# Kernel tuning notes

Hardware: AMD Instinct MI355X
Metric: run time of the kernel (lower is better)

The kernel has to match this reference:

```python
import jax, jax.numpy as jnp
import numpy as np

N_NODE = 100000
N_EDGE = 1600000
D_IN = 128
D_OUT = 128
D_EDGE = 32
EPS = 1e-10


def setup_inputs() -> dict:
    key = jax.random.key(0)
    ks = jax.random.split(key, 8)
    x = jax.random.normal(ks[0], (N_NODE, D_IN), dtype=jnp.float32)
    edge_list = jax.random.randint(ks[1], (N_EDGE, 2), 0, N_NODE, dtype=jnp.int32)
    edge_weights = jax.random.uniform(ks[2], (N_EDGE,), dtype=jnp.float32)
    edge_feature = jax.random.normal(ks[3], (N_EDGE, D_EDGE), dtype=jnp.float32)
    W_lin = jax.random.normal(ks[4], (D_OUT, D_IN), dtype=jnp.float32) * 0.05
    b_lin = jnp.zeros((D_OUT,), dtype=jnp.float32)
    W_edge = jax.random.normal(ks[5], (D_IN, D_EDGE), dtype=jnp.float32) * 0.05
    b_edge = jnp.zeros((D_IN,), dtype=jnp.float32)
    return {"x": x, "edge_list": edge_list, "edge_weights": edge_weights,
            "edge_feature": edge_feature, "W_lin": W_lin, "b_lin": b_lin,
            "W_edge": W_edge, "b_edge": b_edge}


def reference(x, edge_list, edge_weights, edge_feature, W_lin, b_lin, W_edge, b_edge):
    N = x.shape[0]
    src = edge_list[:, 0]  # node_in
    dst = edge_list[:, 1]  # node_out
    loops = jnp.arange(N, dtype=src.dtype)
    node_in = jnp.concatenate([src, loops])    # [E+N]
    node_out = jnp.concatenate([dst, loops])   # [E+N]
    ew = jnp.concatenate([edge_weights, jnp.ones((N,), x.dtype)])  # [E+N]
    # weighted degrees (torchdrug convention) + 1 for self loops
    deg_in = jax.ops.segment_sum(edge_weights, src, num_segments=N) + 1.0
    deg_out = jax.ops.segment_sum(edge_weights, dst, num_segments=N) + 1.0
    # symmetric degree normalization per (extended) edge
    w = ew / (jnp.sqrt(deg_in[node_in] * deg_out[node_out]) + EPS)  # [E+N]
    # sparse adj.T @ x: gather source features, scale, scatter-add to dest
    update = jax.ops.segment_sum(w[:, None] * x[node_in], node_out, num_segments=N)
    # edge-feature contribution (zeros for self loops)
    e = edge_feature @ W_edge.T + b_edge                        # [E, D_IN]
    e = jnp.concatenate([e, jnp.zeros((N, e.shape[1]), x.dtype)])
    update = update + jax.ops.segment_sum(w[:, None] * e, node_out, num_segments=N)
    # combine: linear + relu
    return jax.nn.relu(update @ W_lin.T + b_lin)
```

## Files before the change

kernel.cpp:

```cpp
#include <hip/hip_runtime.h>

#define N_NODES 100000
#define N_EDGES 1600000
#define D 128
#define DE 32
#define SCAN_CHUNK 1024
#define N_CHUNKS ((N_NODES + SCAN_CHUNK - 1) / SCAN_CHUNK)


__device__ inline float bfu(ushort u) {
  return __uint_as_float((unsigned)u << 16);
}
__device__ inline unsigned pk_bf2(float lo, float hi) {
  unsigned a = __float_as_uint(lo), b = __float_as_uint(hi);
  a = (a + 0x7FFFu + ((a >> 16) & 1)) >> 16;
  b = (b + 0x7FFFu + ((b >> 16) & 1)) >> 16;
  return a | (b << 16);
}

__global__ __launch_bounds__(256) void init_kernel(int* __restrict__ z) {
  int idx = blockIdx.x * 256 + threadIdx.x;
  if (idx < 5 * N_NODES) z[idx] = 0;
}

__global__ __launch_bounds__(256) void pos_kernel(
    const int4* __restrict__ el2, int* __restrict__ cursor,
    int2* __restrict__ pos2) {
  int i = blockIdx.x * 256 + threadIdx.x;
  if (i >= N_EDGES / 2) return;
  int4 e = el2[i];
  int2 p;
  p.x = atomicAdd(&cursor[e.y], 1);
  p.y = atomicAdd(&cursor[e.w], 1);
  pos2[i] = p;
}

__global__ __launch_bounds__(256) void scan1_kernel(
    const int* __restrict__ counts, int* __restrict__ partial,
    int* __restrict__ blocksum) {
  __shared__ int lds[256];
  int t = threadIdx.x;
  int base = blockIdx.x * SCAN_CHUNK + t * 4;
  int c[4];
  int s = 0;
#pragma unroll
  for (int k = 0; k < 4; k++) {
    c[k] = (base + k < N_NODES) ? counts[base + k] : 0;
    s += c[k];
  }
  lds[t] = s;
  __syncthreads();
  for (int off = 1; off < 256; off <<= 1) {
    int tmp = (t >= off) ? lds[t - off] : 0;
    __syncthreads();
    lds[t] += tmp;
    __syncthreads();
  }
  int run = lds[t] - s;
#pragma unroll
  for (int k = 0; k < 4; k++) {
    int v = base + k;
    if (v < N_NODES) partial[v] = run;
    run += c[k];
  }
  if (t == 255) blocksum[blockIdx.x] = lds[255];
}

__global__ __launch_bounds__(128) void scan2_kernel(
    const int* __restrict__ blocksum, int* __restrict__ blockoff) {
  __shared__ int lds[128];
  int t = threadIdx.x;
  int v = (t < N_CHUNKS) ? blocksum[t] : 0;
  lds[t] = v;
  __syncthreads();
  for (int off = 1; off < 128; off <<= 1) {
    int tmp = (t >= off) ? lds[t - off] : 0;
    __syncthreads();
    lds[t] += tmp;
    __syncthreads();
  }
  if (t < N_CHUNKS) blockoff[t] = lds[t] - v;
}

__global__ __launch_bounds__(256) void place_kernel(
    const int4* __restrict__ el2, const float2* __restrict__ ew2,
    const int2* __restrict__ pos2, const int* __restrict__ partial,
    const int* __restrict__ blockoff, float* __restrict__ deg4,
    int4* __restrict__ rec) {
  int i = blockIdx.x * 256 + threadIdx.x;
  if (i >= N_EDGES / 2) return;
  int4 e = el2[i];
  float2 w = ew2[i];
  int2 p = pos2[i];
  int r0 = (threadIdx.x & 3) * N_NODES;
  atomicAdd(&deg4[r0 + e.x], w.x);
  atomicAdd(&deg4[r0 + e.z], w.y);
  int4 rA, rB;
  rA.x = e.x; rA.y = 2 * i;     rA.z = __float_as_int(w.x); rA.w = 0;
  rB.x = e.z; rB.y = 2 * i + 1; rB.z = __float_as_int(w.y); rB.w = 0;
  rec[partial[e.y] + blockoff[e.y >> 10] + p.x] = rA;
  rec[partial[e.w] + blockoff[e.w >> 10] + p.y] = rB;
}

__global__ __launch_bounds__(256) void rdi_kernel(
    const float* __restrict__ deg4, float* __restrict__ rdi) {
  int v = blockIdx.x * 256 + threadIdx.x;
  if (v >= N_NODES) return;
  rdi[v] = rsqrtf(1.f + deg4[v] + deg4[N_NODES + v] + deg4[2 * N_NODES + v] +
                  deg4[3 * N_NODES + v]);
}

__global__ __launch_bounds__(256) void xh_kernel(
    const float4* __restrict__ x4, uint4* __restrict__ xh4) {
  int i = blockIdx.x * 256 + threadIdx.x;
  if (i >= N_NODES * D / 8) return;
  float4 f0 = x4[2 * i], f1 = x4[2 * i + 1];
  uint4 o;
  o.x = pk_bf2(f0.x, f0.y);
  o.y = pk_bf2(f0.z, f0.w);
  o.z = pk_bf2(f1.x, f1.y);
  o.w = pk_bf2(f1.z, f1.w);
  xh4[i] = o;
}

template <bool BF16>
__global__ __launch_bounds__(256) void gather_fused_kernel(
    const float* __restrict__ x, const ushort* __restrict__ xh,
    const float* __restrict__ ef, const int* __restrict__ partial,
    const int* __restrict__ blockoff, const int* __restrict__ counts,
    const int4* __restrict__ rec, const float* __restrict__ rdi,
    const float* __restrict__ W_edge, const float* __restrict__ b_edge,
    float* __restrict__ out) {
  __shared__ __align__(16) float we[128 * 36];
  __shared__ float beS[128];
  int t = threadIdx.x;
#pragma unroll
  for (int i = 0; i < 4; ++i) {
    int f = t + i * 256;
    int r = f >> 3, kq = f & 7;
    *(float4*)&we[r * 36 + 4 * kq] = *(const float4*)&W_edge[r * DE + 4 * kq];
  }
  if (t < 128) beS[t] = b_edge[t];
  __syncthreads();

  int wid = t >> 6, lane = t & 63;
  int v = blockIdx.x * 4 + wid;
  if (v >= N_NODES) return;
  int start = partial[v] + blockoff[v >> 10];
  int cnt = counts[v];

  float A0 = 0.f, A1 = 0.f, B0 = 0.f, B1 = 0.f;
  float C0 = 0.f, C1 = 0.f, E0 = 0.f, E1 = 0.f;
  float ga = 0.f, gb = 0.f, dsum = 0.f, wsv = 0.f;

  for (int base = 0; base < cnt; base += 64) {
    int nb = cnt - base;
    if (nb > 64) nb = 64;
    int s_l = 0, e_l = 0;
    float w_l = 0.f;
    if (lane < nb) {
      int4 r = rec[start + base + lane];
      s_l = r.x;
      e_l = r.y;
      float wraw = __int_as_float(r.z);
      w_l = wraw * rdi[r.x];
      dsum += wraw;
      wsv += w_l;
    }
    int i = 0;
    for (; i + 4 <= nb; i += 4) {
      int s0 = __shfl(s_l, i), s1 = __shfl(s_l, i + 1);
      int s2 = __shfl(s_l, i + 2), s3 = __shfl(s_l, i + 3);
      float w0 = __shfl(w_l, i), w1 = __shfl(w_l, i + 1);
      float w2 = __shfl(w_l, i + 2), w3 = __shfl(w_l, i + 3);
      int selA = i + (lane >> 5), selB = i + 2 + (lane >> 5);
      int eA = __shfl(e_l, selA), eB = __shfl(e_l, selB);
      float wA = __shfl(w_l, selA), wB = __shfl(w_l, selB);
      ga = fmaf(wA,
                __builtin_nontemporal_load(&ef[(size_t)eA * DE + (lane & 31)]),
                ga);
      gb = fmaf(wB,
                __builtin_nontemporal_load(&ef[(size_t)eB * DE + (lane & 31)]),
                gb);
      if (BF16) {
        const ushort* p0 = xh + (size_t)s0 * D;
        const ushort* p1 = xh + (size_t)s1 * D;
        const ushort* p2 = xh + (size_t)s2 * D;
        const ushort* p3 = xh + (size_t)s3 * D;
        A0 = fmaf(w0, bfu(p0[lane]), A0);
        A1 = fmaf(w0, bfu(p0[lane + 64]), A1);
        B0 = fmaf(w1, bfu(p1[lane]), B0);
        B1 = fmaf(w1, bfu(p1[lane + 64]), B1);
        C0 = fmaf(w2, bfu(p2[lane]), C0);
        C1 = fmaf(w2, bfu(p2[lane + 64]), C1);
        E0 = fmaf(w3, bfu(p3[lane]), E0);
        E1 = fmaf(w3, bfu(p3[lane + 64]), E1);
      } else {
        const float* p0 = x + (size_t)s0 * D;
        const float* p1 = x + (size_t)s1 * D;
        const float* p2 = x + (size_t)s2 * D;
        const float* p3 = x + (size_t)s3 * D;
        A0 = fmaf(w0, p0[lane], A0);
        A1 = fmaf(w0, p0[lane + 64], A1);
        B0 = fmaf(w1, p1[lane], B0);
        B1 = fmaf(w1, p1[lane + 64], B1);
        C0 = fmaf(w2, p2[lane], C0);
        C1 = fmaf(w2, p2[lane + 64], C1);
        E0 = fmaf(w3, p3[lane], E0);
        E1 = fmaf(w3, p3[lane + 64], E1);
      }
    }
    for (; i + 2 <= nb; i += 2) {
      int s0 = __shfl(s_l, i), s1 = __shfl(s_l, i + 1);
      float w0 = __shfl(w_l, i), w1 = __shfl(w_l, i + 1);
      int sel = i + (lane >> 5);
      int eE = __shfl(e_l, sel);
      float wE = __shfl(w_l, sel);
      ga = fmaf(wE,
                __builtin_nontemporal_load(&ef[(size_t)eE * DE + (lane & 31)]),
                ga);
      if (BF16) {
        const ushort* p0 = xh + (size_t)s0 * D;
        const ushort* p1 = xh + (size_t)s1 * D;
        A0 = fmaf(w0, bfu(p0[lane]), A0);
        A1 = fmaf(w0, bfu(p0[lane + 64]), A1);
        B0 = fmaf(w1, bfu(p1[lane]), B0);
        B1 = fmaf(w1, bfu(p1[lane + 64]), B1);
      } else {
        const float* p0 = x + (size_t)s0 * D;
        const float* p1 = x + (size_t)s1 * D;
        A0 = fmaf(w0, p0[lane], A0);
        A1 = fmaf(w0, p0[lane + 64], A1);
        B0 = fmaf(w1, p1[lane], B0);
        B1 = fmaf(w1, p1[lane + 64], B1);
      }
    }
    if (i < nb) {
      int s0 = __shfl(s_l, i);
      float w0 = __shfl(w_l, i);
      int eA = __shfl(e_l, i);
      if (lane < DE)
        ga = fmaf(w0, __builtin_nontemporal_load(&ef[(size_t)eA * DE + lane]),
                  ga);
      if (BF16) {
        const ushort* p0 = xh + (size_t)s0 * D;
        A0 = fmaf(w0, bfu(p0[lane]), A0);
        A1 = fmaf(w0, bfu(p0[lane + 64]), A1);
      } else {
        const float* p0 = x + (size_t)s0 * D;
        A0 = fmaf(w0, p0[lane], A0);
        A1 = fmaf(w0, p0[lane + 64], A1);
      }
    }
  }
  float a0 = (A0 + B0) + (C0 + E0);
  float a1 = (A1 + B1) + (C1 + E1);
#pragma unroll
  for (int off = 32; off; off >>= 1) {
    dsum += __shfl_xor(dsum, off);
    wsv += __shfl_xor(wsv, off);
  }
  float rdo = rsqrtf(1.f + dsum);
  float gk = ga + gb;
  gk = gk + __shfl(gk, (lane + 32) & 63);

  size_t ro = (size_t)v * D;
  float xs0, xs1;
  if (BF16) {
    xs0 = bfu(xh[ro + lane]);
    xs1 = bfu(xh[ro + lane + 64]);
  } else {
    xs0 = x[ro + lane];
    xs1 = x[ro + lane + 64];
  }
  float wselfp = rdi[v];
  float s0 = a0 + wselfp * xs0 + wsv * beS[lane];
  float s1 = a1 + wselfp * xs1 + wsv * beS[lane + 64];
#pragma unroll
  for (int kq = 0; kq < 8; ++kq) {
    float4 w0 = *(const float4*)&we[lane * 36 + 4 * kq];
    float4 w1 = *(const float4*)&we[(lane + 64) * 36 + 4 * kq];
    float g0 = __shfl(gk, 4 * kq);
    float g1 = __shfl(gk, 4 * kq + 1);
    float g2 = __shfl(gk, 4 * kq + 2);
    float g3 = __shfl(gk, 4 * kq + 3);
    s0 += g0 * w0.x + g1 * w0.y + g2 * w0.z + g3 * w0.w;
    s1 += g0 * w1.x + g1 * w1.y + g2 * w1.z + g3 * w1.w;
  }
  out[ro + lane] = rdo * s0;
  out[ro + lane + 64] = rdo * s1;
}

__global__ __launch_bounds__(256, 3) void gemm2_kernel(
    const float* __restrict__ W_lin, const float* __restrict__ b_lin,
    float* __restrict__ out) {
  __shared__ __align__(16) float xs[128 * 32];
  __shared__ __align__(16) float wl[128 * 32];
  int t = threadIdx.x;
  int tn = t & 15, tm = t >> 4;
  int m0 = 4 * tm, n0 = 4 * tn;
  int vbase = blockIdx.x * 128;
  float acc[8][8] = {};

  for (int ks = 0; ks < D; ks += 32) {
    __syncthreads();
#pragma unroll
    for (int i = 0; i < 4; ++i) {
      int f = t + i * 256;
      int r = f >> 3, kq = f & 7;
      int sw = (4 * kq) ^ (4 * ((r >> 2) & 7));
      float4 xv = make_float4(0.f, 0.f, 0.f, 0.f);
      if (vbase + r < N_NODES)
        xv = *(const float4*)&out[(size_t)(vbase + r) * D + ks + 4 * kq];
      *(float4*)&xs[r * 32 + sw] = xv;
      *(float4*)&wl[r * 32 + sw] = *(const float4*)&W_lin[r * D + ks + 4 * kq];
    }
    __syncthreads();
#pragma unroll 1
    for (int kq = 0; kq < 8; ++kq) {
      int sa = (4 * kq) ^ (4 * (tm & 7));
      int sb = (4 * kq) ^ (4 * (tn & 7));
      float4 a[8];
#pragma unroll
      for (int i = 0; i < 4; ++i) {
        a[i] = *(const float4*)&xs[(m0 + i) * 32 + sa];
        a[4 + i] = *(const float4*)&xs[(m0 + 64 + i) * 32 + sa];
      }
#pragma unroll
      for (int j = 0; j < 8; ++j) {
        int rj = (j < 4) ? (n0 + j) : (n0 + 60 + j);
        float4 b = *(const float4*)&wl[rj * 32 + sb];
#pragma unroll
        for (int i = 0; i < 8; ++i) {
          acc[i][j] += a[i].x * b.x + a[i].y * b.y + a[i].z * b.z +
                       a[i].w * b.w;
        }
      }
    }
  }

  float bl[8];
#pragma unroll
  for (int j = 0; j < 4; ++j) {
    bl[j] = b_lin[n0 + j];
    bl[4 + j] = b_lin[n0 + 64 + j];
  }
#pragma unroll
  for (int i = 0; i < 8; ++i) {
    int m = vbase + m0 + (i < 4 ? i : 64 + i - 4);
    if (m >= N_NODES) continue;
    float4 o0, o1;
    o0.x = fmaxf(acc[i][0] + bl[0], 0.f);
    o0.y = fmaxf(acc[i][1] + bl[1], 0.f);
    o0.z = fmaxf(acc[i][2] + bl[2], 0.f);
    o0.w = fmaxf(acc[i][3] + bl[3], 0.f);
    o1.x = fmaxf(acc[i][4] + bl[4], 0.f);
    o1.y = fmaxf(acc[i][5] + bl[5], 0.f);
    o1.z = fmaxf(acc[i][6] + bl[6], 0.f);
    o1.w = fmaxf(acc[i][7] + bl[7], 0.f);
    *(float4*)&out[(size_t)m * D + n0] = o0;
    *(float4*)&out[(size_t)m * D + n0 + 64] = o1;
  }
}

extern "C" void kernel_launch(void* const* d_in, const int* in_sizes, int n_in,
                              void* d_out, int out_size, void* d_ws,
                              size_t ws_size, hipStream_t stream) {
  const float* x      = (const float*)d_in[0];
  const int*   el     = (const int*)d_in[1];
  const float* ew     = (const float*)d_in[2];
  const float* ef     = (const float*)d_in[3];
  const float* W_lin  = (const float*)d_in[4];
  const float* b_lin  = (const float*)d_in[5];
  const float* W_edge = (const float*)d_in[6];
  const float* b_edge = (const float*)d_in[7];

  float* outp = (float*)d_out;

  char* base = (char*)d_ws;
  size_t off = 0;
  int4* rec      = (int4*)(base + off); off += (size_t)N_EDGES * 16;
  ushort* xh     = (ushort*)(base + off); off += (size_t)N_NODES * D * 2;
  int*  pos      = (int*)(base + off);  off += (size_t)N_EDGES * 4;
  float* deg4    = (float*)(base + off); off += (size_t)4 * N_NODES * 4;
  int*  cursor   = (int*)(base + off);  off += (size_t)N_NODES * 4;
  int*  partial  = (int*)(base + off);  off += (size_t)N_NODES * 4;
  int*  blocksum = (int*)(base + off);  off += 512;
  int*  blockoff = (int*)(base + off);  off += 512;
  float* rdi     = (float*)(base + off); off += (size_t)N_NODES * 4;
  const size_t REQ_FAST = off;
  bool fast = (ws_size >= REQ_FAST);
  if (!fast) {
    off = (size_t)N_EDGES * 16;
    pos      = (int*)(base + off);  off += (size_t)N_EDGES * 4;
    deg4     = (float*)(base + off); off += (size_t)4 * N_NODES * 4;
    cursor   = (int*)(base + off);  off += (size_t)N_NODES * 4;
    partial  = (int*)(base + off);  off += (size_t)N_NODES * 4;
    blocksum = (int*)(base + off);  off += 512;
    blockoff = (int*)(base + off);  off += 512;
    rdi      = (float*)(base + off); off += (size_t)N_NODES * 4;
    xh       = nullptr;
  }

  hipLaunchKernelGGL(init_kernel, dim3((5 * N_NODES + 255) / 256), dim3(256),
                     0, stream, (int*)deg4);
  hipLaunchKernelGGL(pos_kernel, dim3((N_EDGES / 2 + 255) / 256), dim3(256), 0,
                     stream, (const int4*)el, cursor, (int2*)pos);
  hipLaunchKernelGGL(scan1_kernel, dim3(N_CHUNKS), dim3(256), 0, stream,
                     cursor, partial, blocksum);
  hipLaunchKernelGGL(scan2_kernel, dim3(1), dim3(128), 0, stream, blocksum,
                     blockoff);
  hipLaunchKernelGGL(place_kernel, dim3((N_EDGES / 2 + 255) / 256), dim3(256),
                     0, stream, (const int4*)el, (const float2*)ew,
                     (const int2*)pos, partial, blockoff, deg4, rec);
  hipLaunchKernelGGL(rdi_kernel, dim3((N_NODES + 255) / 256), dim3(256), 0,
                     stream, deg4, rdi);
  if (fast) {
    hipLaunchKernelGGL(xh_kernel, dim3((N_NODES * D / 8 + 255) / 256),
                       dim3(256), 0, stream, (const float4*)x, (uint4*)xh);
    hipLaunchKernelGGL(gather_fused_kernel<true>, dim3((N_NODES + 3) / 4),
                       dim3(256), 0, stream, x, xh, ef, partial, blockoff,
                       cursor, rec, rdi, W_edge, b_edge, outp);
  } else {
    hipLaunchKernelGGL(gather_fused_kernel<false>, dim3((N_NODES + 3) / 4),
                       dim3(256), 0, stream, x, xh, ef, partial, blockoff,
                       cursor, rec, rdi, W_edge, b_edge, outp);
  }
  hipLaunchKernelGGL(gemm2_kernel, dim3((N_NODES + 127) / 128), dim3(256), 0,
                     stream, W_lin, b_lin, outp);
}
```

Before: 391.0 us.

## Restructure gather loop with uniform record loads and packed column pairs

The gather kernel drops the per-64-edge chunking, where records were loaded per lane and broadcast by shuffles. Each wave now reads the edge records directly at a wave-uniform address, made uniform with readfirstlane so the compiler can use scalar loads. Each lane now owns two adjacent columns, so bf16 and fp32 rows are fetched as one 32-bit or 64-bit load per lane instead of two separate loads. The edge-feature projection epilogue uses a transposed W_edge in LDS plus a per-wave LDS buffer of aggregated edge features, replacing 32 shuffles. This cuts shuffle and instruction overhead and widens memory accesses, at the cost of redundant record loads per lane and an LDS write/read handoff within each wave.

```diff
diff --git a/kernel.cpp b/kernel.cpp
--- a/kernel.cpp
+++ b/kernel.cpp
@@ -8,8 +8,11 @@
 #define N_CHUNKS ((N_NODES + SCAN_CHUNK - 1) / SCAN_CHUNK)
 
 
-__device__ inline float bfu(ushort u) {
-  return __uint_as_float((unsigned)u << 16);
+__device__ inline float bflo(unsigned u) {
+  return __uint_as_float(u << 16);
+}
+__device__ inline float bfhi(unsigned u) {
+  return __uint_as_float(u & 0xFFFF0000u);
 }
 __device__ inline unsigned pk_bf2(float lo, float hi) {
   unsigned a = __float_as_uint(lo), b = __float_as_uint(hi);
@@ -131,14 +134,13 @@
     const int4* __restrict__ rec, const float* __restrict__ rdi,
     const float* __restrict__ W_edge, const float* __restrict__ b_edge,
     float* __restrict__ out) {
-  __shared__ __align__(16) float we[128 * 36];
+  __shared__ __align__(16) float wet[DE * 132];
   __shared__ float beS[128];
+  __shared__ float gbuf[4][DE];
   int t = threadIdx.x;
-#pragma unroll
-  for (int i = 0; i < 4; ++i) {
-    int f = t + i * 256;
-    int r = f >> 3, kq = f & 7;
-    *(float4*)&we[r * 36 + 4 * kq] = *(const float4*)&W_edge[r * DE + 4 * kq];
+  for (int idx = t; idx < D * DE; idx += 256) {
+    int d = idx >> 5, k = idx & 31;
+    wet[k * 132 + d] = W_edge[idx];
   }
   if (t < 128) beS[t] = b_edge[t];
   __syncthreads();
@@ -146,149 +148,107 @@
   int wid = t >> 6, lane = t & 63;
   int v = blockIdx.x * 4 + wid;
   if (v >= N_NODES) return;
-  int start = partial[v] + blockoff[v >> 10];
-  int cnt = counts[v];
+  int start = __builtin_amdgcn_readfirstlane(partial[v] + blockoff[v >> 10]);
+  int cnt = __builtin_amdgcn_readfirstlane(counts[v]);
 
   float A0 = 0.f, A1 = 0.f, B0 = 0.f, B1 = 0.f;
   float C0 = 0.f, C1 = 0.f, E0 = 0.f, E1 = 0.f;
   float ga = 0.f, gb = 0.f, dsum = 0.f, wsv = 0.f;
-
-  for (int base = 0; base < cnt; base += 64) {
-    int nb = cnt - base;
-    if (nb > 64) nb = 64;
-    int s_l = 0, e_l = 0;
-    float w_l = 0.f;
-    if (lane < nb) {
-      int4 r = rec[start + base + lane];
-      s_l = r.x;
-      e_l = r.y;
-      float wraw = __int_as_float(r.z);
-      w_l = wraw * rdi[r.x];
-      dsum += wraw;
-      wsv += w_l;
+  int lane31 = lane & 31;
+  bool lowhalf = lane < 32;
+
+  int i = 0;
+  for (; i + 4 <= cnt; i += 4) {
+    int4 r0 = rec[start + i];
+    int4 r1 = rec[start + i + 1];
+    int4 r2 = rec[start + i + 2];
+    int4 r3 = rec[start + i + 3];
+    float wr0 = __int_as_float(r0.z), wr1 = __int_as_float(r1.z);
+    float wr2 = __int_as_float(r2.z), wr3 = __int_as_float(r3.z);
+    float w0 = wr0 * rdi[r0.x];
+    float w1 = wr1 * rdi[r1.x];
+    float w2 = wr2 * rdi[r2.x];
+    float w3 = wr3 * rdi[r3.x];
+    dsum += (wr0 + wr1) + (wr2 + wr3);
+    wsv += (w0 + w1) + (w2 + w3);
+    float wA = lowhalf ? w0 : w1;
+    int eA = lowhalf ? r0.y : r1.y;
+    float wB = lowhalf ? w2 : w3;
+    int eB = lowhalf ? r2.y : r3.y;
+    ga = fmaf(wA, __builtin_nontemporal_load(&ef[(size_t)eA * DE + lane31]),
+              ga);
+    gb = fmaf(wB, __builtin_nontemporal_load(&ef[(size_t)eB * DE + lane31]),
+              gb);
+    if (BF16) {
+      unsigned u0 = ((const unsigned*)(xh + (size_t)r0.x * D))[lane];
+      unsigned u1 = ((const unsigned*)(xh + (size_t)r1.x * D))[lane];
+      unsigned u2 = ((const unsigned*)(xh + (size_t)r2.x * D))[lane];
+      unsigned u3 = ((const unsigned*)(xh + (size_t)r3.x * D))[lane];
+      A0 = fmaf(w0, bflo(u0), A0); A1 = fmaf(w0, bfhi(u0), A1);
+      B0 = fmaf(w1, bflo(u1), B0); B1 = fmaf(w1, bfhi(u1), B1);
+      C0 = fmaf(w2, bflo(u2), C0); C1 = fmaf(w2, bfhi(u2), C1);
+      E0 = fmaf(w3, bflo(u3), E0); E1 = fmaf(w3, bfhi(u3), E1);
+    } else {
+      float2 u0 = ((const float2*)(x + (size_t)r0.x * D))[lane];
+      float2 u1 = ((const float2*)(x + (size_t)r1.x * D))[lane];
+      float2 u2 = ((const float2*)(x + (size_t)r2.x * D))[lane];
+      float2 u3 = ((const float2*)(x + (size_t)r3.x * D))[lane];
+      A0 = fmaf(w0, u0.x, A0); A1 = fmaf(w0, u0.y, A1);
+      B0 = fmaf(w1, u1.x, B0); B1 = fmaf(w1, u1.y, B1);
+      C0 = fmaf(w2, u2.x, C0); C1 = fmaf(w2, u2.y, C1);
+      E0 = fmaf(w3, u3.x, E0); E1 = fmaf(w3, u3.y, E1);
     }
-    int i = 0;
-    for (; i + 4 <= nb; i += 4) {
-      int s0 = __shfl(s_l, i), s1 = __shfl(s_l, i + 1);
-      int s2 = __shfl(s_l, i + 2), s3 = __shfl(s_l, i + 3);
-      float w0 = __shfl(w_l, i), w1 = __shfl(w_l, i + 1);
-      float w2 = __shfl(w_l, i + 2), w3 = __shfl(w_l, i + 3);
-      int selA = i + (lane >> 5), selB = i + 2 + (lane >> 5);
-      int eA = __shfl(e_l, selA), eB = __shfl(e_l, selB);
-      float wA = __shfl(w_l, selA), wB = __shfl(w_l, selB);
-      ga = fmaf(wA,
-                __builtin_nontemporal_load(&ef[(size_t)eA * DE + (lane & 31)]),
+  }
+  for (; i < cnt; ++i) {
+    int4 r0 = rec[start + i];
+    float wr0 = __int_as_float(r0.z);
+    float w0 = wr0 * rdi[r0.x];
+    dsum += wr0;
+    wsv += w0;
+    if (lowhalf)
+      ga = fmaf(w0, __builtin_nontemporal_load(&ef[(size_t)r0.y * DE + lane31]),
                 ga);
-      gb = fmaf(wB,
-                __builtin_nontemporal_load(&ef[(size_t)eB * DE + (lane & 31)]),
-                gb);
-      if (BF16) {
-        const ushort* p0 = xh + (size_t)s0 * D;
-        const ushort* p1 = xh + (size_t)s1 * D;
-        const ushort* p2 = xh + (size_t)s2 * D;
-        const ushort* p3 = xh + (size_t)s3 * D;
-        A0 = fmaf(w0, bfu(p0[lane]), A0);
-        A1 = fmaf(w0, bfu(p0[lane + 64]), A1);
-        B0 = fmaf(w1, bfu(p1[lane]), B0);
-        B1 = fmaf(w1, bfu(p1[lane + 64]), B1);
-        C0 = fmaf(w2, bfu(p2[lane]), C0);
-        C1 = fmaf(w2, bfu(p2[lane + 64]), C1);
-        E0 = fmaf(w3, bfu(p3[lane]), E0);
-        E1 = fmaf(w3, bfu(p3[lane + 64]), E1);
-      } else {
-        const float* p0 = x + (size_t)s0 * D;
-        const float* p1 = x + (size_t)s1 * D;
-        const float* p2 = x + (size_t)s2 * D;
-        const float* p3 = x + (size_t)s3 * D;
-        A0 = fmaf(w0, p0[lane], A0);
-        A1 = fmaf(w0, p0[lane + 64], A1);
-        B0 = fmaf(w1, p1[lane], B0);
-        B1 = fmaf(w1, p1[lane + 64], B1);
-        C0 = fmaf(w2, p2[lane], C0);
-        C1 = fmaf(w2, p2[lane + 64], C1);
-        E0 = fmaf(w3, p3[lane], E0);
-        E1 = fmaf(w3, p3[lane + 64], E1);
-      }
-    }
-    for (; i + 2 <= nb; i += 2) {
-      int s0 = __shfl(s_l, i), s1 = __shfl(s_l, i + 1);
-      float w0 = __shfl(w_l, i), w1 = __shfl(w_l, i + 1);
-      int sel = i + (lane >> 5);
-      int eE = __shfl(e_l, sel);
-      float wE = __shfl(w_l, sel);
-      ga = fmaf(wE,
-                __builtin_nontemporal_load(&ef[(size_t)eE * DE + (lane & 31)]),
-                ga);
-      if (BF16) {
-        const ushort* p0 = xh + (size_t)s0 * D;
-        const ushort* p1 = xh + (size_t)s1 * D;
-        A0 = fmaf(w0, bfu(p0[lane]), A0);
-        A1 = fmaf(w0, bfu(p0[lane + 64]), A1);
-        B0 = fmaf(w1, bfu(p1[lane]), B0);
-        B1 = fmaf(w1, bfu(p1[lane + 64]), B1);
-      } else {
-        const float* p0 = x + (size_t)s0 * D;
-        const float* p1 = x + (size_t)s1 * D;
-        A0 = fmaf(w0, p0[lane], A0);
-        A1 = fmaf(w0, p0[lane + 64], A1);
-        B0 = fmaf(w1, p1[lane], B0);
-        B1 = fmaf(w1, p1[lane + 64], B1);
-      }
-    }
-    if (i < nb) {
-      int s0 = __shfl(s_l, i);
-      float w0 = __shfl(w_l, i);
-      int eA = __shfl(e_l, i);
-      if (lane < DE)
-        ga = fmaf(w0, __builtin_nontemporal_load(&ef[(size_t)eA * DE + lane]),
-                  ga);
-      if (BF16) {
-        const ushort* p0 = xh + (size_t)s0 * D;
-        A0 = fmaf(w0, bfu(p0[lane]), A0);
-        A1 = fmaf(w0, bfu(p0[lane + 64]), A1);
-      } else {
-        const float* p0 = x + (size_t)s0 * D;
-        A0 = fmaf(w0, p0[lane], A0);
-        A1 = fmaf(w0, p0[lane + 64], A1);
-      }
+    if (BF16) {
+      unsigned u0 = ((const unsigned*)(xh + (size_t)r0.x * D))[lane];
+      A0 = fmaf(w0, bflo(u0), A0);
+      A1 = fmaf(w0, bfhi(u0), A1);
+    } else {
+      float2 u0 = ((const float2*)(x + (size_t)r0.x * D))[lane];
+      A0 = fmaf(w0, u0.x, A0);
+      A1 = fmaf(w0, u0.y, A1);
     }
   }
   float a0 = (A0 + B0) + (C0 + E0);
   float a1 = (A1 + B1) + (C1 + E1);
-#pragma unroll
-  for (int off = 32; off; off >>= 1) {
-    dsum += __shfl_xor(dsum, off);
-    wsv += __shfl_xor(wsv, off);
-  }
+
   float rdo = rsqrtf(1.f + dsum);
-  float gk = ga + gb;
-  gk = gk + __shfl(gk, (lane + 32) & 63);
+  float gfull = ga + gb;
+  gfull += __shfl(gfull, (lane + 32) & 63);
+  if (lowhalf) gbuf[wid][lane] = gfull;
 
   size_t ro = (size_t)v * D;
   float xs0, xs1;
   if (BF16) {
-    xs0 = bfu(xh[ro + lane]);
-    xs1 = bfu(xh[ro + lane + 64]);
+    unsigned u = ((const unsigned*)(xh + ro))[lane];
+    xs0 = bflo(u);
+    xs1 = bfhi(u);
   } else {
-    xs0 = x[ro + lane];
-    xs1 = x[ro + lane + 64];
-  }
-  float wselfp = rdi[v];
-  float s0 = a0 + wselfp * xs0 + wsv * beS[lane];
-  float s1 = a1 + wselfp * xs1 + wsv * beS[lane + 64];
-#pragma unroll
-  for (int kq = 0; kq < 8; ++kq) {
-    float4 w0 = *(const float4*)&we[lane * 36 + 4 * kq];
-    float4 w1 = *(const float4*)&we[(lane + 64) * 36 + 4 * kq];
-    float g0 = __shfl(gk, 4 * kq);
-    float g1 = __shfl(gk, 4 * kq + 1);
-    float g2 = __shfl(gk, 4 * kq + 2);
-    float g3 = __shfl(gk, 4 * kq + 3);
-    s0 += g0 * w0.x + g1 * w0.y + g2 * w0.z + g3 * w0.w;
-    s1 += g0 * w1.x + g1 * w1.y + g2 * w1.z + g3 * w1.w;
-  }
-  out[ro + lane] = rdo * s0;
-  out[ro + lane + 64] = rdo * s1;
+    float2 u = ((const float2*)(x + ro))[lane];
+    xs0 = u.x;
+    xs1 = u.y;
+  }
+  float rdiv = rdi[v];
+  float2 be = *(const float2*)&beS[2 * lane];
+  float s0 = a0 + rdiv * xs0 + wsv * be.x;
+  float s1 = a1 + rdiv * xs1 + wsv * be.y;
+#pragma unroll
+  for (int k = 0; k < DE; ++k) {
+    float gk = gbuf[wid][k];
+    float2 wv = *(const float2*)&wet[k * 132 + 2 * lane];
+    s0 = fmaf(gk, wv.x, s0);
+    s1 = fmaf(gk, wv.y, s1);
+  }
+  ((float2*)(out + ro))[lane] = make_float2(rdo * s0, rdo * s1);
 }
 
 __global__ __launch_bounds__(256, 3) void gemm2_kernel(
```

Result: slower. 410.0 us (+4.9%).

## Merge bf16 conversion into pos kernel and widen gather loads with unroll-8

Applied to the files above, without the earlier changes.

The x-to-bf16 conversion now runs as extra blocks of the edge-position kernel, which removes one launch and lets the two independent jobs overlap. The gather loop now processes 8 neighbours per iteration instead of 4, with four independent edge-feature accumulators. Each lane loads two adjacent columns in one 32-bit bf16 pair (or a float2) instead of two scattered 16-bit or 32-bit loads. The interleaved column ownership is undone with shuffles before the epilogue. This gives more memory-level parallelism and fewer load instructions, at the cost of higher register pressure and a few extra shuffles.

```diff
diff --git a/kernel.cpp b/kernel.cpp
--- a/kernel.cpp
+++ b/kernel.cpp
@@ -6,10 +6,15 @@
 #define DE 32
 #define SCAN_CHUNK 1024
 #define N_CHUNKS ((N_NODES + SCAN_CHUNK - 1) / SCAN_CHUNK)
-
-
-__device__ inline float bfu(ushort u) {
-  return __uint_as_float((unsigned)u << 16);
+#define POS_BLOCKS (N_EDGES / 2 / 256)
+#define XH_BLOCKS (N_NODES * D / 8 / 256)
+
+
+__device__ inline float bflo(unsigned u) {
+  return __uint_as_float(u << 16);
+}
+__device__ inline float bfhi(unsigned u) {
+  return __uint_as_float(u & 0xFFFF0000u);
 }
 __device__ inline unsigned pk_bf2(float lo, float hi) {
   unsigned a = __float_as_uint(lo), b = __float_as_uint(hi);
@@ -23,16 +28,30 @@
   if (idx < 5 * N_NODES) z[idx] = 0;
 }
 
-__global__ __launch_bounds__(256) void pos_kernel(
+__global__ __launch_bounds__(256) void pos_xh_kernel(
     const int4* __restrict__ el2, int* __restrict__ cursor,
-    int2* __restrict__ pos2) {
-  int i = blockIdx.x * 256 + threadIdx.x;
-  if (i >= N_EDGES / 2) return;
-  int4 e = el2[i];
-  int2 p;
-  p.x = atomicAdd(&cursor[e.y], 1);
-  p.y = atomicAdd(&cursor[e.w], 1);
-  pos2[i] = p;
+    int2* __restrict__ pos2, const float4* __restrict__ x4,
+    uint4* __restrict__ xh4) {
+  int b = blockIdx.x;
+  if (b < POS_BLOCKS) {
+    int i = b * 256 + threadIdx.x;
+    if (i >= N_EDGES / 2) return;
+    int4 e = el2[i];
+    int2 p;
+    p.x = atomicAdd(&cursor[e.y], 1);
+    p.y = atomicAdd(&cursor[e.w], 1);
+    pos2[i] = p;
+  } else {
+    int i = (b - POS_BLOCKS) * 256 + threadIdx.x;
+    if (i >= N_NODES * D / 8) return;
+    float4 f0 = x4[2 * i], f1 = x4[2 * i + 1];
+    uint4 o;
+    o.x = pk_bf2(f0.x, f0.y);
+    o.y = pk_bf2(f0.z, f0.w);
+    o.z = pk_bf2(f1.x, f1.y);
+    o.w = pk_bf2(f1.z, f1.w);
+    xh4[i] = o;
+  }
 }
 
 __global__ __launch_bounds__(256) void scan1_kernel(
@@ -110,19 +129,6 @@
                   deg4[3 * N_NODES + v]);
 }
 
-__global__ __launch_bounds__(256) void xh_kernel(
-    const float4* __restrict__ x4, uint4* __restrict__ xh4) {
-  int i = blockIdx.x * 256 + threadIdx.x;
-  if (i >= N_NODES * D / 8) return;
-  float4 f0 = x4[2 * i], f1 = x4[2 * i + 1];
-  uint4 o;
-  o.x = pk_bf2(f0.x, f0.y);
-  o.y = pk_bf2(f0.z, f0.w);
-  o.z = pk_bf2(f1.x, f1.y);
-  o.w = pk_bf2(f1.z, f1.w);
-  xh4[i] = o;
-}
-
 template <bool BF16>
 __global__ __launch_bounds__(256) void gather_fused_kernel(
     const float* __restrict__ x, const ushort* __restrict__ xh,
@@ -148,10 +154,12 @@
   if (v >= N_NODES) return;
   int start = partial[v] + blockoff[v >> 10];
   int cnt = counts[v];
+  int lane31 = lane & 31;
+  bool lowhalf = lane < 32;
 
   float A0 = 0.f, A1 = 0.f, B0 = 0.f, B1 = 0.f;
   float C0 = 0.f, C1 = 0.f, E0 = 0.f, E1 = 0.f;
-  float ga = 0.f, gb = 0.f, dsum = 0.f, wsv = 0.f;
+  float ga = 0.f, gb = 0.f, gc = 0.f, gd = 0.f, dsum = 0.f, wsv = 0.f;
 
   for (int base = 0; base < cnt; base += 64) {
     int nb = cnt - base;
@@ -168,88 +176,99 @@
       wsv += w_l;
     }
     int i = 0;
-    for (; i + 4 <= nb; i += 4) {
-      int s0 = __shfl(s_l, i), s1 = __shfl(s_l, i + 1);
+    for (; i + 8 <= nb; i += 8) {
+      int s0 = __shfl(s_l, i + 0), s1 = __shfl(s_l, i + 1);
       int s2 = __shfl(s_l, i + 2), s3 = __shfl(s_l, i + 3);
-      float w0 = __shfl(w_l, i), w1 = __shfl(w_l, i + 1);
+      int s4 = __shfl(s_l, i + 4), s5 = __shfl(s_l, i + 5);
+      int s6 = __shfl(s_l, i + 6), s7 = __shfl(s_l, i + 7);
+      float w0 = __shfl(w_l, i + 0), w1 = __shfl(w_l, i + 1);
       float w2 = __shfl(w_l, i + 2), w3 = __shfl(w_l, i + 3);
-      int selA = i + (lane >> 5), selB = i + 2 + (lane >> 5);
-      int eA = __shfl(e_l, selA), eB = __shfl(e_l, selB);
-      float wA = __shfl(w_l, selA), wB = __shfl(w_l, selB);
-      ga = fmaf(wA,
-                __builtin_nontemporal_load(&ef[(size_t)eA * DE + (lane & 31)]),
+      float w4 = __shfl(w_l, i + 4), w5 = __shfl(w_l, i + 5);
+      float w6 = __shfl(w_l, i + 6), w7 = __shfl(w_l, i + 7);
+      int hh = lane >> 5;
+      int eA = __shfl(e_l, i + 0 + hh), eB = __shfl(e_l, i + 2 + hh);
+      int eC = __shfl(e_l, i + 4 + hh), eD = __shfl(e_l, i + 6 + hh);
+      float wA = lowhalf ? w0 : w1, wB = lowhalf ? w2 : w3;
+      float wC = lowhalf ? w4 : w5, wD = lowhalf ? w6 : w7;
+      ga = fmaf(wA, __builtin_nontemporal_load(&ef[(size_t)eA * DE + lane31]),
                 ga);
-      gb = fmaf(wB,
-                __builtin_nontemporal_load(&ef[(size_t)eB * DE + (lane & 31)]),
+      gb = fmaf(wB, __builtin_nontemporal_load(&ef[(size_t)eB * DE + lane31]),
                 gb);
+      gc = fmaf(wC, __builtin_nontemporal_load(&ef[(size_t)eC * DE + lane31]),
+                gc);
+      gd = fmaf(wD, __builtin_nontemporal_load(&ef[(size_t)eD * DE + lane31]),
+                gd);
       if (BF16) {
-        const ushort* p0 = xh + (size_t)s0 * D;
-        const ushort* p1 = xh + (size_t)s1 * D;
-        const ushort* p2 = xh + (size_t)s2 * D;
-        const ushort* p3 = xh + (size_t)s3 * D;
-        A0 = fmaf(w0, bfu(p0[lane]), A0);
-        A1 = fmaf(w0, bfu(p0[lane + 64]), A1);
-        B0 = fmaf(w1, bfu(p1[lane]), B0);
-        B1 = fmaf(w1, bfu(p1[lane + 64]), B1);
-        C0 = fmaf(w2, bfu(p2[lane]), C0);
-        C1 = fmaf(w2, bfu(p2[lane + 64]), C1);
-        E0 = fmaf(w3, bfu(p3[lane]), E0);
-        E1 = fmaf(w3, bfu(p3[lane + 64]), E1);
+        unsigned u0 = ((const unsigned*)(xh + (size_t)s0 * D))[lane];
+        unsigned u1 = ((const unsigned*)(xh + (size_t)s1 * D))[lane];
+        unsigned u2 = ((const unsigned*)(xh + (size_t)s2 * D))[lane];
+        unsigned u3 = ((const unsigned*)(xh + (size_t)s3 * D))[lane];
+        unsigned u4 = ((const unsigned*)(xh + (size_t)s4 * D))[lane];
+        unsigned u5 = ((const unsigned*)(xh + (size_t)s5 * D))[lane];
+        unsigned u6 = ((const unsigned*)(xh + (size_t)s6 * D))[lane];
+        unsigned u7 = ((const unsigned*)(xh + (size_t)s7 * D))[lane];
+        A0 = fmaf(w0, bflo(u0), A0); A1 = fmaf(w0, bfhi(u0), A1);
+        B0 = fmaf(w1, bflo(u1), B0); B1 = fmaf(w1, bfhi(u1), B1);
+        C0 = fmaf(w2, bflo(u2), C0); C1 = fmaf(w2, bfhi(u2), C1);
+        E0 = fmaf(w3, bflo(u3), E0); E1 = fmaf(w3, bfhi(u3), E1);
+        A0 = fmaf(w4, bflo(u4), A0); A1 = fmaf(w4, bfhi(u4), A1);
+        B0 = fmaf(w5, bflo(u5), B0); B1 = fmaf(w5, bfhi(u5), B1);
+        C0 = fmaf(w6, bflo(u6), C0); C1 = fmaf(w6, bfhi(u6), C1);
+        E0 = fmaf(w7, bflo(u7), E0); E1 = fmaf(w7, bfhi(u7), E1);
       } else {
-        const float* p0 = x + (size_t)s0 * D;
-        const float* p1 = x + (size_t)s1 * D;
-        const float* p2 = x + (size_t)s2 * D;
-        const float* p3 = x + (size_t)s3 * D;
-        A0 = fmaf(w0, p0[lane], A0);
-        A1 = fmaf(w0, p0[lane + 64], A1);
-        B0 = fmaf(w1, p1[lane], B0);
-        B1 = fmaf(w1, p1[lane + 64], B1);
-        C0 = fmaf(w2, p2[lane], C0);
-        C1 = fmaf(w2, p2[lane + 64], C1);
-        E0 = fmaf(w3, p3[lane], E0);
-        E1 = fmaf(w3, p3[lane + 64], E1);
+        float2 u0 = ((const float2*)(x + (size_t)s0 * D))[lane];
+        float2 u1 = ((const float2*)(x + (size_t)s1 * D))[lane];
+        float2 u2 = ((const float2*)(x + (size_t)s2 * D))[lane];
+        float2 u3 = ((const float2*)(x + (size_t)s3 * D))[lane];
+        float2 u4 = ((const float2*)(x + (size_t)s4 * D))[lane];
+        float2 u5 = ((const float2*)(x + (size_t)s5 * D))[lane];
+        float2 u6 = ((const float2*)(x + (size_t)s6 * D))[lane];
+        float2 u7 = ((const float2*)(x + (size_t)s7 * D))[lane];
+        A0 = fmaf(w0, u0.x, A0); A1 = fmaf(w0, u0.y, A1);
+        B0 = fmaf(w1, u1.x, B0); B1 = fmaf(w1, u1.y, B1);
+        C0 = fmaf(w2, u2.x, C0); C1 = fmaf(w2, u2.y, C1);
+        E0 = fmaf(w3, u3.x, E0); E1 = fmaf(w3, u3.y, E1);
+        A0 = fmaf(w4, u4.x, A0); A1 = fmaf(w4, u4.y, A1);
+        B0 = fmaf(w5, u5.x, B0); B1 = fmaf(w5, u5.y, B1);
+        C0 = fmaf(w6, u6.x, C0); C1 = fmaf(w6, u6.y, C1);
+        E0 = fmaf(w7, u7.x, E0); E1 = fmaf(w7, u7.y, E1);
       }
     }
     for (; i + 2 <= nb; i += 2) {
       int s0 = __shfl(s_l, i), s1 = __shfl(s_l, i + 1);
       float w0 = __shfl(w_l, i), w1 = __shfl(w_l, i + 1);
-      int sel = i + (lane >> 5);
-      int eE = __shfl(e_l, sel);
-      float wE = __shfl(w_l, sel);
-      ga = fmaf(wE,
-                __builtin_nontemporal_load(&ef[(size_t)eE * DE + (lane & 31)]),
+      int eE = __shfl(e_l, i + (lane >> 5));
+      float wE = lowhalf ? w0 : w1;
+      ga = fmaf(wE, __builtin_nontemporal_load(&ef[(size_t)eE * DE + lane31]),
                 ga);
       if (BF16) {
-        const ushort* p0 = xh + (size_t)s0 * D;
-        const ushort* p1 = xh + (size_t)s1 * D;
-        A0 = fmaf(w0, bfu(p0[lane]), A0);
-        A1 = fmaf(w0, bfu(p0[lane + 64]), A1);
-        B0 = fmaf(w1, bfu(p1[lane]), B0);
-        B1 = fmaf(w1, bfu(p1[lane + 64]), B1);
+        unsigned u0 = ((const unsigned*)(xh + (size_t)s0 * D))[lane];
+        unsigned u1 = ((const unsigned*)(xh + (size_t)s1 * D))[lane];
+        A0 = fmaf(w0, bflo(u0), A0); A1 = fmaf(w0, bfhi(u0), A1);
+        B0 = fmaf(w1, bflo(u1), B0); B1 = fmaf(w1, bfhi(u1), B1);
       } else {
-        const float* p0 = x + (size_t)s0 * D;
-        const float* p1 = x + (size_t)s1 * D;
-        A0 = fmaf(w0, p0[lane], A0);
-        A1 = fmaf(w0, p0[lane + 64], A1);
-        B0 = fmaf(w1, p1[lane], B0);
-        B1 = fmaf(w1, p1[lane + 64], B1);
+        float2 u0 = ((const float2*)(x + (size_t)s0 * D))[lane];
+        float2 u1 = ((const float2*)(x + (size_t)s1 * D))[lane];
+        A0 = fmaf(w0, u0.x, A0); A1 = fmaf(w0, u0.y, A1);
+        B0 = fmaf(w1, u1.x, B0); B1 = fmaf(w1, u1.y, B1);
       }
     }
     if (i < nb) {
       int s0 = __shfl(s_l, i);
       float w0 = __shfl(w_l, i);
       int eA = __shfl(e_l, i);
-      if (lane < DE)
-        ga = fmaf(w0, __builtin_nontemporal_load(&ef[(size_t)eA * DE + lane]),
+      if (lowhalf)
+        ga = fmaf(w0,
+                  __builtin_nontemporal_load(&ef[(size_t)eA * DE + lane31]),
                   ga);
       if (BF16) {
-        const ushort* p0 = xh + (size_t)s0 * D;
-        A0 = fmaf(w0, bfu(p0[lane]), A0);
-        A1 = fmaf(w0, bfu(p0[lane + 64]), A1);
+        unsigned u0 = ((const unsigned*)(xh + (size_t)s0 * D))[lane];
+        A0 = fmaf(w0, bflo(u0), A0);
+        A1 = fmaf(w0, bfhi(u0), A1);
       } else {
-        const float* p0 = x + (size_t)s0 * D;
-        A0 = fmaf(w0, p0[lane], A0);
-        A1 = fmaf(w0, p0[lane + 64], A1);
+        float2 u0 = ((const float2*)(x + (size_t)s0 * D))[lane];
+        A0 = fmaf(w0, u0.x, A0);
+        A1 = fmaf(w0, u0.y, A1);
       }
     }
   }
@@ -261,21 +280,29 @@
     wsv += __shfl_xor(wsv, off);
   }
   float rdo = rsqrtf(1.f + dsum);
-  float gk = ga + gb;
-  gk = gk + __shfl(gk, (lane + 32) & 63);
+  float gfull = (ga + gb) + (gc + gd);
+  gfull += __shfl(gfull, (lane + 32) & 63);
+  float gk = gfull;
+
+  int half = lane >> 1;
+  float v0 = __shfl(a0, half), v1 = __shfl(a1, half);
+  float accLo = (lane & 1) ? v1 : v0;
+  float q0 = __shfl(a0, 32 + half), q1 = __shfl(a1, 32 + half);
+  float accHi = (lane & 1) ? q1 : q0;
 
   size_t ro = (size_t)v * D;
   float xs0, xs1;
   if (BF16) {
-    xs0 = bfu(xh[ro + lane]);
-    xs1 = bfu(xh[ro + lane + 64]);
+    xs0 = bflo((unsigned)xh[ro + lane] << 16) , xs1 = 0.f;
+    xs0 = __uint_as_float((unsigned)xh[ro + lane] << 16);
+    xs1 = __uint_as_float((unsigned)xh[ro + lane + 64] << 16);
   } else {
     xs0 = x[ro + lane];
     xs1 = x[ro + lane + 64];
   }
-  float wselfp = rdi[v];
-  float s0 = a0 + wselfp * xs0 + wsv * beS[lane];
-  float s1 = a1 + wselfp * xs1 + wsv * beS[lane + 64];
+  float rdiv = rdi[v];
+  float s0 = accLo + rdiv * xs0 + wsv * beS[lane];
+  float s1 = accHi + rdiv * xs1 + wsv * beS[lane + 64];
 #pragma unroll
   for (int kq = 0; kq < 8; ++kq) {
     float4 w0 = *(const float4*)&we[lane * 36 + 4 * kq];
@@ -404,8 +431,10 @@
 
   hipLaunchKernelGGL(init_kernel, dim3((5 * N_NODES + 255) / 256), dim3(256),
                      0, stream, (int*)deg4);
-  hipLaunchKernelGGL(pos_kernel, dim3((N_EDGES / 2 + 255) / 256), dim3(256), 0,
-                     stream, (const int4*)el, cursor, (int2*)pos);
+  hipLaunchKernelGGL(pos_xh_kernel,
+                     dim3(fast ? POS_BLOCKS + XH_BLOCKS : POS_BLOCKS),
+                     dim3(256), 0, stream, (const int4*)el, cursor, (int2*)pos,
+                     (const float4*)x, (uint4*)xh);
   hipLaunchKernelGGL(scan1_kernel, dim3(N_CHUNKS), dim3(256), 0, stream,
                      cursor, partial, blocksum);
   hipLaunchKernelGGL(scan2_kernel, dim3(1), dim3(128), 0, stream, blocksum,
@@ -416,8 +445,6 @@
   hipLaunchKernelGGL(rdi_kernel, dim3((N_NODES + 255) / 256), dim3(256), 0,
                      stream, deg4, rdi);
   if (fast) {
-    hipLaunchKernelGGL(xh_kernel, dim3((N_NODES * D / 8 + 255) / 256),
-                       dim3(256), 0, stream, (const float4*)x, (uint4*)xh);
     hipLaunchKernelGGL(gather_fused_kernel<true>, dim3((N_NODES + 3) / 4),
                        dim3(256), 0, stream, x, xh, ef, partial, blockoff,
                        cursor, rec, rdi, W_edge, b_edge, outp);
```

Measured after the change: 392.9 us. About the same (+0.5%).
